# Kernel tuning notes

Hardware: AMD Instinct MI355X
Metric: run time of the kernel (lower is better)

## Reference

```python
import jax, jax.numpy as jnp
import numpy as np

B, C, H, W, K = 16, 64, 256, 256, 7
PAD = K // 2
HID = C // 4


def setup_inputs() -> dict:
    key = jax.random.key(0)
    k_x, k_w1, k_w2 = jax.random.split(key, 3)
    x = jax.random.normal(k_x, (B, C, H, W), dtype=jnp.float32)
    # Linear weights stored as (in, out); torch stores (out, in) but math is identical.
    w1 = jax.random.normal(k_w1, (C, HID), dtype=jnp.float32) * (1.0 / np.sqrt(C))
    b1 = jnp.zeros((HID,), dtype=jnp.float32)
    w2 = jax.random.normal(k_w2, (HID, C * K * K), dtype=jnp.float32) * (1.0 / np.sqrt(HID))
    b2 = jnp.zeros((C * K * K,), dtype=jnp.float32)
    return {"x": x, "w1": w1, "b1": b1, "w2": w2, "b2": b2}


def reference(x, w1, b1, w2, b2):
    b, c, h, w = x.shape
    # GAP -> (B, C)
    pooled = jnp.mean(x, axis=(2, 3))
    # MLP kernel generator: Linear -> exact GELU (torch nn.GELU default) -> Linear -> sigmoid
    hdn = jax.nn.gelu(pooled @ w1 + b1, approximate=False)
    weights = jax.nn.sigmoid(hdn @ w2 + b2).reshape(b * c, 1, K, K)  # OIHW, depthwise
    # reflect pad spatial dims, merge batch into group dim
    xp = jnp.pad(x, ((0, 0), (0, 0), (PAD, PAD), (PAD, PAD)), mode="reflect")
    xp = xp.reshape(1, b * c, h + 2 * PAD, w + 2 * PAD)
    out = jax.lax.conv_general_dilated(
        xp, weights,
        window_strides=(1, 1), padding="VALID",
        dimension_numbers=("NCHW", "OIHW", "NCHW"),
        feature_group_count=b * c,
    )
    return out.reshape(b, c, h, w)
```

## Files before the change

### kernel.cpp

```cpp
#include <hip/hip_runtime.h>
#include <math.h>

#define BATCH 16
#define CH    64
#define HDIM  256
#define WDIM  256
#define HW    65536
#define KS    7
#define HIDN  16
#define COUT  3136
#define NPLANE 1024

__global__ __launch_bounds__(512) void gap_kernel(const float* __restrict__ x,
                                                  float* __restrict__ pooled) {
    const int p = blockIdx.x;
    const float4* xv = (const float4*)(x + (size_t)p * HW);
    const int t = threadIdx.x;
    float s = 0.f;
    #pragma unroll 4
    for (int i = t; i < 16384; i += 512) {
        float4 a = xv[i];
        s += (a.x + a.y) + (a.z + a.w);
    }
    #pragma unroll
    for (int off = 32; off > 0; off >>= 1) s += __shfl_down(s, off);
    __shared__ float sp[8];
    const int wid = t >> 6, lane = t & 63;
    if (lane == 0) sp[wid] = s;
    __syncthreads();
    if (t == 0) {
        float tot = 0.f;
        #pragma unroll
        for (int i = 0; i < 8; ++i) tot += sp[i];
        pooled[p] = tot * (1.0f / 65536.0f);
    }
}

__global__ __launch_bounds__(256) void mlp_kernel(const float* __restrict__ pooled,
                                                  const float* __restrict__ w1,
                                                  const float* __restrict__ b1,
                                                  const float* __restrict__ w2,
                                                  const float* __restrict__ b2,
                                                  float* __restrict__ wout) {
    __shared__ float s_pool[NPLANE];
    __shared__ float s_hdn[BATCH * HIDN];
    const int t = threadIdx.x;
    for (int i = t; i < NPLANE; i += 256) s_pool[i] = pooled[i];
    __syncthreads();
    {
        const int i = t >> 4, j = t & 15;
        float acc = b1[j];
        #pragma unroll
        for (int c = 0; c < 64; ++c) acc += s_pool[i * 64 + c] * w1[c * HIDN + j];
        s_hdn[t] = 0.5f * acc * (1.0f + erff(acc * 0.70710678118654752f));
    }
    __syncthreads();
    const int o = blockIdx.x * 256 + t;
    const int i = o / COUT;
    const int j = o - i * COUT;
    float acc = b2[j];
    #pragma unroll
    for (int h = 0; h < HIDN; ++h) acc += s_hdn[i * HIDN + h] * w2[h * COUT + j];
    wout[o] = 1.0f / (1.0f + expf(-acc));
}

#define TLX 128
#define TLY 64
#define INX 134
#define INY 70
#define LDSS 136

__global__ __launch_bounds__(256, 3) void conv_kernel(const float* __restrict__ x,
                                                      const float* __restrict__ wts,
                                                      float* __restrict__ out) {
    __shared__ float s_in[INY * LDSS];
    __shared__ float s_w[49];
    const int p = blockIdx.z;
    const size_t pbase = (size_t)p * HW;
    const int gx0 = blockIdx.x * TLX - 3;
    const int gy0 = blockIdx.y * TLY - 3;
    const int t = threadIdx.x;

    if (t < 49) s_w[t] = wts[p * 49 + t];

    for (int idx = t; idx < INY * INX; idx += 256) {
        const int r = idx / INX;
        const int c = idx - r * INX;
        int gy = gy0 + r;
        gy = gy < 0 ? -gy : (gy > 255 ? 510 - gy : gy);
        int gx = gx0 + c;
        gx = gx < 0 ? -gx : (gx > 255 ? 510 - gx : gx);
        s_in[r * LDSS + c] = x[pbase + (size_t)gy * WDIM + gx];
    }
    __syncthreads();

    float w[49];
    #pragma unroll
    for (int i = 0; i < 49; ++i) w[i] = s_w[i];

    const int tx4 = (t & 31) * 4;
    const int ty  = (t >> 5) * 8;

    float acc[32];
    #pragma unroll
    for (int i = 0; i < 32; ++i) acc[i] = 0.f;

    #pragma unroll
    for (int r = 0; r < 14; ++r) {
        const float* rp = &s_in[(ty + r) * LDSS + tx4];
        const float4 v0 = *(const float4*)(rp);
        const float4 v1 = *(const float4*)(rp + 4);
        const float4 v2 = *(const float4*)(rp + 8);
        const float row[12] = {v0.x, v0.y, v0.z, v0.w,
                               v1.x, v1.y, v1.z, v1.w,
                               v2.x, v2.y, v2.z, v2.w};
        #pragma unroll
        for (int o = 0; o < 8; ++o) {
            const int ky = r - o;
            if (ky < 0 || ky > 6) continue;
            #pragma unroll
            for (int kx = 0; kx < 7; ++kx) {
                const float wv = w[ky * 7 + kx];
                acc[o * 4 + 0] += wv * row[kx + 0];
                acc[o * 4 + 1] += wv * row[kx + 1];
                acc[o * 4 + 2] += wv * row[kx + 2];
                acc[o * 4 + 3] += wv * row[kx + 3];
            }
        }
    }

    const int oy0 = blockIdx.y * TLY + ty;
    const int ox  = blockIdx.x * TLX + tx4;
    #pragma unroll
    for (int o = 0; o < 8; ++o) {
        const float4 v = make_float4(acc[o * 4 + 0], acc[o * 4 + 1],
                                     acc[o * 4 + 2], acc[o * 4 + 3]);
        *(float4*)&out[pbase + (size_t)(oy0 + o) * WDIM + ox] = v;
    }
}

extern "C" void kernel_launch(void* const* d_in, const int* in_sizes, int n_in,
                              void* d_out, int out_size, void* d_ws, size_t ws_size,
                              hipStream_t stream) {
    const float* x  = (const float*)d_in[0];
    const float* w1 = (const float*)d_in[1];
    const float* b1 = (const float*)d_in[2];
    const float* w2 = (const float*)d_in[3];
    const float* b2 = (const float*)d_in[4];
    float* out = (float*)d_out;

    float* pooled = (float*)d_ws;
    float* wts    = pooled + NPLANE;

    gap_kernel<<<NPLANE, 512, 0, stream>>>(x, pooled);
    mlp_kernel<<<(BATCH * COUT) / 256, 256, 0, stream>>>(pooled, w1, b1, w2, b2, wts);
    conv_kernel<<<dim3(WDIM / TLX, HDIM / TLY, NPLANE), 256, 0, stream>>>(x, wts, out);
}
```

Before: 569.2 us.

## Use full-width row tiles with direct global-to-LDS loads and nontemporal stores

Conv tiles now span the full 256-column row with 32 rows, and each wave loads whole rows straight into LDS via global_load_lds, applying reflect only at the row edges. This removes the per-element divide and reflect arithmetic and the register round trip of the old staging loop. Output stores become nontemporal, and occupancy hint rises to 4 blocks. Vertical halo overhead grows with the shorter tile.

```diff
diff --git a/kernel.cpp b/kernel.cpp
--- a/kernel.cpp
+++ b/kernel.cpp
@@ -10,6 +10,8 @@
 #define HIDN  16
 #define COUT  3136
 #define NPLANE 1024
+
+typedef float vfloat4 __attribute__((ext_vector_type(4)));
 
 __global__ __launch_bounds__(512) void gap_kernel(const float* __restrict__ x,
                                                   float* __restrict__ pooled) {
@@ -64,33 +66,47 @@
     wout[o] = 1.0f / (1.0f + expf(-acc));
 }
 
-#define TLX 128
-#define TLY 64
-#define INX 134
-#define INY 70
-#define LDSS 136
+#define TLY  32
+#define INY  38
+#define LDSS 264
 
-__global__ __launch_bounds__(256, 3) void conv_kernel(const float* __restrict__ x,
+#define GLDS4(gsrc, ldst) __builtin_amdgcn_global_load_lds(                     \
+    (const __attribute__((address_space(1))) void*)(gsrc),                      \
+    (__attribute__((address_space(3))) void*)(ldst), 4, 0, 0)
+
+__global__ __launch_bounds__(256, 4) void conv_kernel(const float* __restrict__ x,
                                                       const float* __restrict__ wts,
                                                       float* __restrict__ out) {
     __shared__ float s_in[INY * LDSS];
     __shared__ float s_w[49];
-    const int p = blockIdx.z;
+    const int t    = threadIdx.x;
+    const int lane = t & 63;
+    const int wid  = t >> 6;
+    const int p    = blockIdx.y;
     const size_t pbase = (size_t)p * HW;
-    const int gx0 = blockIdx.x * TLX - 3;
-    const int gy0 = blockIdx.y * TLY - 3;
-    const int t = threadIdx.x;
+    const int gy0 = blockIdx.x * TLY - 3;
 
     if (t < 49) s_w[t] = wts[p * 49 + t];
 
-    for (int idx = t; idx < INY * INX; idx += 256) {
-        const int r = idx / INX;
-        const int c = idx - r * INX;
+    for (int r0 = wid; r0 < INY; r0 += 4) {
+        const int r = __builtin_amdgcn_readfirstlane(r0);
         int gy = gy0 + r;
         gy = gy < 0 ? -gy : (gy > 255 ? 510 - gy : gy);
-        int gx = gx0 + c;
-        gx = gx < 0 ? -gx : (gx > 255 ? 510 - gx : gx);
-        s_in[r * LDSS + c] = x[pbase + (size_t)gy * WDIM + gx];
+        const float* srow = x + pbase + ((size_t)gy << 8);
+        float* lrow = &s_in[r * LDSS];
+        {
+            int gx = lane - 3;
+            gx = gx < 0 ? -gx : gx;
+            GLDS4(srow + gx, lrow);
+        }
+        GLDS4(srow + (64  - 3) + lane, lrow + 64);
+        GLDS4(srow + (128 - 3) + lane, lrow + 128);
+        GLDS4(srow + (192 - 3) + lane, lrow + 192);
+        if (lane < 8) {
+            int gx = 253 + lane;
+            gx = gx > 255 ? 510 - gx : gx;
+            GLDS4(srow + gx, lrow + 256);
+        }
     }
     __syncthreads();
 
@@ -98,8 +114,8 @@
     #pragma unroll
     for (int i = 0; i < 49; ++i) w[i] = s_w[i];
 
-    const int tx4 = (t & 31) * 4;
-    const int ty  = (t >> 5) * 8;
+    const int tx4 = lane * 4;
+    const int ty  = wid * 8;
 
     float acc[32];
     #pragma unroll
@@ -129,13 +145,13 @@
         }
     }
 
-    const int oy0 = blockIdx.y * TLY + ty;
-    const int ox  = blockIdx.x * TLX + tx4;
+    const int oy0 = blockIdx.x * TLY + ty;
     #pragma unroll
     for (int o = 0; o < 8; ++o) {
-        const float4 v = make_float4(acc[o * 4 + 0], acc[o * 4 + 1],
-                                     acc[o * 4 + 2], acc[o * 4 + 3]);
-        *(float4*)&out[pbase + (size_t)(oy0 + o) * WDIM + ox] = v;
+        vfloat4 v = {acc[o * 4 + 0], acc[o * 4 + 1],
+                     acc[o * 4 + 2], acc[o * 4 + 3]};
+        __builtin_nontemporal_store(v,
+            (vfloat4*)&out[pbase + (size_t)(oy0 + o) * WDIM + tx4]);
     }
 }
 
@@ -154,5 +170,5 @@
 
     gap_kernel<<<NPLANE, 512, 0, stream>>>(x, pooled);
     mlp_kernel<<<(BATCH * COUT) / 256, 256, 0, stream>>>(pooled, w1, b1, w2, b2, wts);
-    conv_kernel<<<dim3(WDIM / TLX, HDIM / TLY, NPLANE), 256, 0, stream>>>(x, wts, out);
+    conv_kernel<<<dim3(HDIM / TLY, NPLANE), 256, 0, stream>>>(x, wts, out);
 }
```

After: 564.6 us. Within noise of the previous version (-0.8%).
